# Kernel optimization log

Measured on AMD Instinct MI355X. Metric: run time of the kernel, lower is better.

The kernel has to match this reference:

```python
import jax, jax.numpy as jnp
import numpy as np

B, CHANS, SAMPLES = 256, 22, 1125
DEPTH, CD1, CD2, KT = 9, 24, 9, 75
K_CHEB, N_CHEB_LAYERS, AVEPOOL = 3, 5, 5
W1 = SAMPLES - KT + 1          # 1051 after valid (1,75) conv
WP = W1 // AVEPOOL             # 210 after avgpool
FEAT = CD2 * WP                # 1890 -> fc1


def _bn(x, p, eps=1e-5):
    # eval-mode BatchNorm2d over channel axis 1; p rows = [gamma, beta, mean, var]
    g, b, m, v = p
    s = (1, -1, 1, 1)
    return (x - m.reshape(s)) / jnp.sqrt(v.reshape(s) + eps) * g.reshape(s) + b.reshape(s)


def _normalize_A(A, lmax=2.0):
    A = jax.nn.relu(A)
    n = A.shape[0]
    I = jnp.eye(n, dtype=A.dtype)
    A = A * (1.0 - I)            # zero diagonal
    A = A + A.T                  # symmetrize
    d = jnp.sum(A, axis=1)
    dis = 1.0 / jnp.sqrt(d + 1e-10)
    L = I - dis[:, None] * A * dis[None, :]
    return 2.0 * L / lmax - I


def _forward(x, channel_weight, tconv1_w, bn1, tconv2_w, bn2, da_w, da_b,
             cconv1_w, bn3, A, A_mask, cheby_W, cheby_b, cconv2_w, bn4,
             fc1_w, fc1_b, mlp_w1, mlp_b1, mlp_w2, mlp_b2):
    dn = ('NCHW', 'OIHW', 'NCHW')
    # lead weighting: (B,1,C,S) x (H,1,C) -> (B,H,C,S)
    x = jnp.einsum('bdcw,hdc->bhcw', x, channel_weight)
    # time_conv: pointwise 1x1 + BN + depthwise (1,KT) + BN + GELU
    x = jnp.einsum('bicw,oi->bocw', x, tconv1_w)
    x = _bn(x, bn1)
    x = jax.lax.conv_general_dilated(x, tconv2_w.reshape(CD1, 1, 1, KT), (1, 1),
                                     'VALID', feature_group_count=CD1,
                                     dimension_numbers=dn)
    x = jax.nn.gelu(_bn(x, bn2), approximate=False)
    # EEGDepthAttention: avg over chans, (7,1) conv on depth axis, softmax over depth
    xp = jnp.mean(x, axis=2, keepdims=True)        # (B,CD1,1,W1)
    xt = jnp.swapaxes(xp, 1, 2)                    # (B,1,CD1,W1)
    y = jax.lax.conv_general_dilated(xt, da_w.reshape(1, 1, 7, 1), (1, 1),
                                     ((3, 3), (0, 0)), dimension_numbers=dn)
    y = jax.nn.softmax(y + da_b.reshape(1, 1, 1, 1), axis=-2)
    x = jnp.swapaxes(y, 1, 2) * CHANS * x          # (B,CD1,C,W1)
    # channel conv part1: 1x1 + BN -> (B,CD2,C,W1)
    x = _bn(jnp.einsum('bicw,oi->bocw', x, cconv1_w), bn3)
    # normalized Laplacian from pruned learnable adjacency
    L = _normalize_A(A * jax.nn.sigmoid(A_mask))
    I = jnp.eye(CHANS, dtype=L.dtype)
    adjs = [I, L, 2.0 * (L @ L) - I][:K_CHEB]      # Chebyshev T_0..T_2
    b_, f_, c_, w_ = x.shape
    xr = jnp.transpose(x, (0, 3, 1, 2)).reshape(b_ * w_, f_, c_)  # (N,F,C)
    for l in range(N_CHEB_LAYERS):
        out = jnp.zeros_like(xr)
        for k in range(K_CHEB):
            out = out + jnp.einsum('cd,nfd,fo->noc', adjs[k], xr, cheby_W[l, k]) \
                      + cheby_b[l, k][None, :, None]
        xr = jax.nn.relu(out)
    x = jnp.transpose(xr.reshape(b_, w_, f_, c_), (0, 2, 3, 1))   # (B,CD2,C,W1)
    # channel conv part2: depthwise (CHANS,1) + BN + GELU -> (B,CD2,1,W1)
    x = jnp.einsum('bfcw,fc->bfw', x, cconv2_w)[:, :, None, :]
    x = jax.nn.gelu(_bn(x, bn4), approximate=False)
    # avgpool kernel/stride AVEPOOL on time; dropout is identity at eval
    x = x[..., :WP * AVEPOOL].reshape(b_, CD2, 1, WP, AVEPOOL).mean(-1)
    x = x.reshape(b_, -1)                           # (B,FEAT)
    x = x @ fc1_w + fc1_b                           # (B,5)
    x = jax.nn.elu(x @ mlp_w1 + mlp_b1) @ mlp_w2 + mlp_b2
    return jax.nn.softmax(x, axis=1)


def setup_inputs() -> dict:
    key = jax.random.key(0)
    ks = iter(jax.random.split(key, 40))

    def randn(shape, s=1.0):
        return jax.random.normal(next(ks), shape, jnp.float32) * s

    def bn_p(c):
        return jnp.stack([jax.random.uniform(next(ks), (c,)) * 0.5 + 0.75,
                          randn((c,), 0.1), randn((c,), 0.1),
                          jax.random.uniform(next(ks), (c,)) * 0.5 + 0.75])

    return {
        'x': randn((B, 1, CHANS, SAMPLES)),
        'channel_weight': randn((DEPTH, 1, CHANS), 0.3),
        'tconv1_w': randn((CD1, DEPTH), 0.3),
        'bn1': bn_p(CD1),
        'tconv2_w': randn((CD1, KT), 0.1),
        'bn2': bn_p(CD1),
        'da_w': randn((7,), 0.3),
        'da_b': randn((1,), 0.1),
        'cconv1_w': randn((CD2, CD1), 0.2),
        'bn3': bn_p(CD2),
        'A': jax.random.uniform(next(ks), (CHANS, CHANS)) * 0.49 + 0.01,
        'A_mask': jnp.ones((CHANS, CHANS), jnp.float32),
        'cheby_W': randn((N_CHEB_LAYERS, K_CHEB, CD2, CD2), 0.3),
        'cheby_b': jnp.zeros((N_CHEB_LAYERS, K_CHEB, CD2), jnp.float32),
        'cconv2_w': randn((CD2, CHANS), 0.2),
        'bn4': bn_p(CD2),
        'fc1_w': randn((FEAT, 5), 0.02),
        'fc1_b': jnp.zeros((5,), jnp.float32),
        'mlp_w1': randn((5, 64), 0.3),
        'mlp_b1': jnp.zeros((64,), jnp.float32),
        'mlp_w2': randn((64, 4), 0.2),
        'mlp_b2': jnp.zeros((4,), jnp.float32),
    }


def reference(x, channel_weight, tconv1_w, bn1, tconv2_w, bn2, da_w, da_b,
              cconv1_w, bn3, A, A_mask, cheby_W, cheby_b, cconv2_w, bn4,
              fc1_w, fc1_b, mlp_w1, mlp_b1, mlp_w2, mlp_b2):
    return _forward(x, channel_weight, tconv1_w, bn1, tconv2_w, bn2, da_w, da_b,
                    cconv1_w, bn3, A, A_mask, cheby_W, cheby_b, cconv2_w, bn4,
                    fc1_w, fc1_b, mlp_w1, mlp_b1, mlp_w2, mlp_b2)
```

## Files before the change

kernel.cpp:

```cpp
#include <hip/hip_runtime.h>
#include <math.h>

#define B_      256
#define CHANS   22
#define SAMPLES 1125
#define DEPTH   9
#define CD1     24
#define CD2     9
#define KT      75
#define W1      1051
#define WP      210
#define FEAT    1890
#define TW      11
#define NT      96

#define WS_W2   0
#define WS_D    528
#define WS_CC1  552
#define WS_B3   768
#define WS_L1   777
#define WS_L2   1261
#define WS_CC2  1745
#define WS_B4   1943
#define WS_BL   1952
#define WS_KT   2000
#define WS_Z    3840

__device__ __forceinline__ float gelu_exact(float v) {
    return 0.5f * v * (1.0f + erff(v * 0.70710678118654752f));
}

__global__ __launch_bounds__(256) void precompute_kernel(
    const float* __restrict__ cw, const float* __restrict__ t1w,
    const float* __restrict__ bn1, const float* __restrict__ t2w,
    const float* __restrict__ bn2, const float* __restrict__ cc1w,
    const float* __restrict__ bn3, const float* __restrict__ A,
    const float* __restrict__ Am, const float* __restrict__ cbB,
    const float* __restrict__ cc2w, const float* __restrict__ bn4,
    float* __restrict__ ws)
{
    __shared__ float a1[CD1], a2[CD1];
    __shared__ float a3[CD2], a4[CD2];
    __shared__ float Ap[484], As[484], dis[22], L1s[484];
    const int tid = threadIdx.x;

    if (tid < CD1) {
        float g1 = bn1[tid], be1 = bn1[24 + tid], m1 = bn1[48 + tid], v1 = bn1[72 + tid];
        a1[tid] = g1 * rsqrtf(v1 + 1e-5f);
        float b1v = be1 - m1 * a1[tid];
        float g2 = bn2[tid], be2 = bn2[24 + tid], m2 = bn2[48 + tid], v2 = bn2[72 + tid];
        a2[tid] = g2 * rsqrtf(v2 + 1e-5f);
        float b2v = be2 - m2 * a2[tid];
        float S = 0.0f;
        for (int k = 0; k < KT; ++k) S += t2w[tid * KT + k];
        ws[WS_D + tid] = a2[tid] * b1v * S + b2v;
    }
    if (tid < CD2) {
        float g3 = bn3[tid], be3 = bn3[9 + tid], m3 = bn3[18 + tid], v3 = bn3[27 + tid];
        a3[tid] = g3 * rsqrtf(v3 + 1e-5f);
        ws[WS_B3 + tid] = be3 - m3 * a3[tid];
        float g4 = bn4[tid], be4 = bn4[9 + tid], m4 = bn4[18 + tid], v4 = bn4[27 + tid];
        a4[tid] = g4 * rsqrtf(v4 + 1e-5f);
        ws[WS_B4 + tid] = be4 - m4 * a4[tid];
    }
    __syncthreads();

    for (int e = tid; e < CD1 * CHANS; e += blockDim.x) {
        int o = e / CHANS, c = e - o * CHANS;
        float m = 0.0f;
        for (int h = 0; h < DEPTH; ++h) m += t1w[o * DEPTH + h] * cw[h * CHANS + c];
        ws[WS_W2 + e] = a2[o] * a1[o] * m;
    }
    for (int e = tid; e < CD2 * CD1; e += blockDim.x) {
        int o = e / CD1;
        ws[WS_CC1 + e] = a3[o] * cc1w[e] * 22.0f;
    }
    for (int e = tid; e < CD2 * CHANS; e += blockDim.x) {
        int f = e / CHANS;
        ws[WS_CC2 + e] = a4[f] * cc2w[e];
    }
    for (int e = tid; e < 45; e += blockDim.x) {
        int l = e / 9, o = e - l * 9;
        ws[WS_BL + e] = cbB[(l * 3 + 0) * 9 + o] + cbB[(l * 3 + 1) * 9 + o] + cbB[(l * 3 + 2) * 9 + o];
    }
    for (int e = tid; e < KT * CD1; e += blockDim.x) {
        int k = e / CD1, o = e - k * CD1;
        ws[WS_KT + e] = t2w[o * KT + k];
    }
    for (int e = tid; e < 484; e += blockDim.x) {
        int c = e / 22, d = e - c * 22;
        float v = A[e] / (1.0f + expf(-Am[e]));
        v = fmaxf(v, 0.0f);
        if (c == d) v = 0.0f;
        Ap[e] = v;
    }
    __syncthreads();
    for (int e = tid; e < 484; e += blockDim.x) {
        int c = e / 22, d = e - c * 22;
        As[e] = Ap[e] + Ap[d * 22 + c];
    }
    __syncthreads();
    if (tid < 22) {
        float s = 0.0f;
        for (int d = 0; d < 22; ++d) s += As[tid * 22 + d];
        dis[tid] = rsqrtf(s + 1e-10f);
    }
    __syncthreads();
    for (int e = tid; e < 484; e += blockDim.x) {
        int c = e / 22, d = e - c * 22;
        float v = -dis[c] * As[e] * dis[d];
        L1s[e] = v;
        ws[WS_L1 + e] = v;
    }
    __syncthreads();
    for (int e = tid; e < 484; e += blockDim.x) {
        int c = e / 22, d = e - c * 22;
        float s = 0.0f;
        for (int k2 = 0; k2 < 22; ++k2) s += L1s[c * 22 + k2] * L1s[k2 * 22 + d];
        ws[WS_L2 + e] = 2.0f * s - (c == d ? 1.0f : 0.0f);
    }
}

#define OXS  0
#define OX   0
#define XSTR 268
#define OG   2948
#define GSTR 532
#define OS   8800
#define XP   9088
#define SMEM_F 9360

__global__ __launch_bounds__(256, 4) void main_kernel(
    const float* __restrict__ x, const float* __restrict__ t2w,
    const float* __restrict__ daw_g, const float* __restrict__ dab_g,
    const float* __restrict__ cbW, float* __restrict__ ws)
{
    __shared__ float sm[SMEM_F];
    const int tid = threadIdx.x;
    const int b = blockIdx.y;
    const int w0 = blockIdx.x * TW;
    const float* cst = ws;
    float* zbuf = ws + WS_Z;

    const int c = tid / TW;
    const int t = tid - c * TW;
    const bool act = (tid < 242);

    for (int e = tid; e < 22 * 88; e += 256) {
        int ch = e / 88, j = e - ch * 88;
        int s = w0 + j;
        float v = 0.0f;
        if (j < 85 && s < SAMPLES) v = x[(b * CHANS + ch) * SAMPLES + s];
        sm[OXS + e] = v;
    }
    __syncthreads();

    if (act) {
        float acc[CD1];
        #pragma unroll
        for (int o = 0; o < CD1; ++o) acc[o] = 0.0f;
        const int xbase = OXS + c * 88 + t;
        #pragma unroll 1
        for (int kc = 0; kc < 9; ++kc) {
            float xw[8];
            #pragma unroll
            for (int j = 0; j < 8; ++j) xw[j] = sm[xbase + kc * 8 + j];
            const float* Ktc = cst + WS_KT + kc * 8 * CD1;
            #pragma unroll
            for (int j = 0; j < 8; ++j) {
                #pragma unroll
                for (int o = 0; o < CD1; ++o)
                    acc[o] = fmaf(Ktc[j * CD1 + o], xw[j], acc[o]);
            }
        }
        {
            float xw[3];
            #pragma unroll
            for (int j = 0; j < 3; ++j) xw[j] = sm[xbase + 72 + j];
            const float* Ktc = cst + WS_KT + 72 * CD1;
            #pragma unroll
            for (int j = 0; j < 3; ++j) {
                #pragma unroll
                for (int o = 0; o < CD1; ++o)
                    acc[o] = fmaf(Ktc[j * CD1 + o], xw[j], acc[o]);
            }
        }
        float g[CD1];
        #pragma unroll
        for (int o = 0; o < CD1; ++o) {
            float w2 = cst[WS_W2 + o * CHANS + c];
            float dd = cst[WS_D + o];
            g[o] = gelu_exact(fmaf(w2, acc[o], dd));
        }
        float4* gp = (float4*)&sm[OG + t * GSTR + c * 24];
        #pragma unroll
        for (int q = 0; q < 6; ++q)
            gp[q] = make_float4(g[4 * q], g[4 * q + 1], g[4 * q + 2], g[4 * q + 3]);
    }
    __syncthreads();

    for (int e = tid; e < CD1 * TW; e += 256) {
        int d = e / TW, tt = e - d * TW;
        float s = 0.0f;
        #pragma unroll
        for (int ch = 0; ch < CHANS; ++ch) s += sm[OG + tt * GSTR + ch * 24 + d];
        sm[XP + e] = s * (1.0f / 22.0f);
    }
    __syncthreads();
    for (int e = tid; e < CD1 * TW; e += 256) {
        int d = e / TW, tt = e - d * TW;
        float y = dab_g[0];
        #pragma unroll
        for (int j = 0; j < 7; ++j) {
            int dd = d + j - 3;
            if (dd >= 0 && dd < CD1) y += daw_g[j] * sm[XP + dd * TW + tt];
        }
        sm[OS + d * 12 + tt] = y;
    }
    __syncthreads();
    if (tid < TW) {
        float mx = -1e30f;
        for (int d = 0; d < CD1; ++d) mx = fmaxf(mx, sm[OS + d * 12 + tid]);
        float sum = 0.0f;
        for (int d = 0; d < CD1; ++d) {
            float e2 = expf(sm[OS + d * 12 + tid] - mx);
            sm[OS + d * 12 + tid] = e2;
            sum += e2;
        }
        float inv = 1.0f / sum;
        for (int d = 0; d < CD1; ++d) sm[OS + d * 12 + tid] *= inv;
    }
    __syncthreads();

    float xo[CD2];
    if (act) {
        float garr[CD1];
        {
            const float4* gp = (const float4*)&sm[OG + t * GSTR + c * 24];
            #pragma unroll
            for (int q = 0; q < 6; ++q) {
                float4 v = gp[q];
                garr[4 * q] = v.x; garr[4 * q + 1] = v.y;
                garr[4 * q + 2] = v.z; garr[4 * q + 3] = v.w;
            }
        }
        #pragma unroll
        for (int o = 0; o < CD2; ++o) xo[o] = cst[WS_B3 + o];
        #pragma unroll
        for (int i = 0; i < CD1; ++i) {
            float s = sm[OS + i * 12 + t];
            float p = s * garr[i];
            #pragma unroll
            for (int o = 0; o < CD2; ++o)
                xo[o] = fmaf(cst[WS_CC1 + o * CD1 + i], p, xo[o]);
        }
        float4* xp = (float4*)&sm[OX + t * XSTR + c * 12];
        xp[0] = make_float4(xo[0], xo[1], xo[2], xo[3]);
        xp[1] = make_float4(xo[4], xo[5], xo[6], xo[7]);
        xp[2] = make_float4(xo[8], 0.0f, 0.0f, 0.0f);
    }
    __syncthreads();

    float t1row[CHANS], t2row[CHANS];
    if (act) {
        #pragma unroll
        for (int d = 0; d < CHANS; ++d) {
            t1row[d] = cst[WS_L1 + c * 22 + d];
            t2row[d] = cst[WS_L2 + c * 22 + d];
        }
    }

    for (int l = 0; l < 5; ++l) {
        float y1[CD2], y2[CD2];
        if (act) {
            #pragma unroll
            for (int o = 0; o < CD2; ++o) { y1[o] = 0.0f; y2[o] = 0.0f; }
            #pragma unroll
            for (int d = 0; d < CHANS; ++d) {
                const float4* p = (const float4*)&sm[OX + t * XSTR + d * 12];
                float4 a = p[0], bb = p[1];
                float x8 = sm[OX + t * XSTR + d * 12 + 8];
                float w1c = t1row[d], w2c = t2row[d];
                y1[0] = fmaf(w1c, a.x, y1[0]);  y2[0] = fmaf(w2c, a.x, y2[0]);
                y1[1] = fmaf(w1c, a.y, y1[1]);  y2[1] = fmaf(w2c, a.y, y2[1]);
                y1[2] = fmaf(w1c, a.z, y1[2]);  y2[2] = fmaf(w2c, a.z, y2[2]);
                y1[3] = fmaf(w1c, a.w, y1[3]);  y2[3] = fmaf(w2c, a.w, y2[3]);
                y1[4] = fmaf(w1c, bb.x, y1[4]); y2[4] = fmaf(w2c, bb.x, y2[4]);
                y1[5] = fmaf(w1c, bb.y, y1[5]); y2[5] = fmaf(w2c, bb.y, y2[5]);
                y1[6] = fmaf(w1c, bb.z, y1[6]); y2[6] = fmaf(w2c, bb.z, y2[6]);
                y1[7] = fmaf(w1c, bb.w, y1[7]); y2[7] = fmaf(w2c, bb.w, y2[7]);
                y1[8] = fmaf(w1c, x8, y1[8]);   y2[8] = fmaf(w2c, x8, y2[8]);
            }
            float out[CD2];
            #pragma unroll
            for (int o = 0; o < CD2; ++o) out[o] = cst[WS_BL + l * 9 + o];
            #pragma unroll
            for (int f = 0; f < CD2; ++f) {
                const float* w0p = cbW + ((l * 3 + 0) * 9 + f) * 9;
                const float* w1p = cbW + ((l * 3 + 1) * 9 + f) * 9;
                const float* w2p = cbW + ((l * 3 + 2) * 9 + f) * 9;
                float xv = xo[f], yv1 = y1[f], yv2 = y2[f];
                #pragma unroll
                for (int o = 0; o < CD2; ++o)
                    out[o] = fmaf(w0p[o], xv, fmaf(w1p[o], yv1, fmaf(w2p[o], yv2, out[o])));
            }
            #pragma unroll
            for (int o = 0; o < CD2; ++o) xo[o] = fmaxf(out[o], 0.0f);
        }
        __syncthreads();
        if (act) {
            float4* xp = (float4*)&sm[OX + t * XSTR + c * 12];
            xp[0] = make_float4(xo[0], xo[1], xo[2], xo[3]);
            xp[1] = make_float4(xo[4], xo[5], xo[6], xo[7]);
            xp[2] = make_float4(xo[8], 0.0f, 0.0f, 0.0f);
        }
        __syncthreads();
    }

    if (tid < CD2 * TW) {
        int f = tid / TW, tt = tid - f * TW;
        float a = cst[WS_B4 + f];
        #pragma unroll
        for (int ch = 0; ch < CHANS; ++ch)
            a = fmaf(cst[WS_CC2 + f * CHANS + ch], sm[OX + tt * XSTR + ch * 12 + f], a);
        float z = gelu_exact(a);
        int w = w0 + tt;
        if (w < W1) zbuf[(b * CD2 + f) * W1 + w] = z;
    }
}

__global__ __launch_bounds__(256) void head_kernel(
    const float* __restrict__ ws, const float* __restrict__ fc1w,
    const float* __restrict__ fc1b, const float* __restrict__ w1,
    const float* __restrict__ b1, const float* __restrict__ w2,
    const float* __restrict__ b2, float* __restrict__ out)
{
    __shared__ float red[5][256];
    __shared__ float l5[5];
    __shared__ float hbuf[64];
    const int tid = threadIdx.x;
    const int b = blockIdx.x;
    const float* zb = ws + WS_Z + b * CD2 * W1;

    float part[5] = {0, 0, 0, 0, 0};
    for (int i = tid; i < FEAT; i += 256) {
        int f = i / WP, t = i - f * WP;
        const float* zp = zb + f * W1 + 5 * t;
        float pooled = 0.2f * (zp[0] + zp[1] + zp[2] + zp[3] + zp[4]);
        #pragma unroll
        for (int j = 0; j < 5; ++j) part[j] = fmaf(pooled, fc1w[i * 5 + j], part[j]);
    }
    #pragma unroll
    for (int j = 0; j < 5; ++j) red[j][tid] = part[j];
    __syncthreads();
    for (int ofs = 128; ofs > 0; ofs >>= 1) {
        if (tid < ofs) {
            #pragma unroll
            for (int j = 0; j < 5; ++j) red[j][tid] += red[j][tid + ofs];
        }
        __syncthreads();
    }
    if (tid < 5) l5[tid] = red[tid][0] + fc1b[tid];
    __syncthreads();
    if (tid < 64) {
        float a = b1[tid];
        #pragma unroll
        for (int j = 0; j < 5; ++j) a = fmaf(l5[j], w1[j * 64 + tid], a);
        hbuf[tid] = (a > 0.0f) ? a : expm1f(a);
    }
    __syncthreads();
    if (tid == 0) {
        float o4[4];
        #pragma unroll
        for (int m = 0; m < 4; ++m) {
            float a = b2[m];
            for (int k = 0; k < 64; ++k) a = fmaf(hbuf[k], w2[k * 4 + m], a);
            o4[m] = a;
        }
        float mx = fmaxf(fmaxf(o4[0], o4[1]), fmaxf(o4[2], o4[3]));
        float s = 0.0f;
        #pragma unroll
        for (int m = 0; m < 4; ++m) { o4[m] = expf(o4[m] - mx); s += o4[m]; }
        float inv = 1.0f / s;
        #pragma unroll
        for (int m = 0; m < 4; ++m) out[b * 4 + m] = o4[m] * inv;
    }
}

extern "C" void kernel_launch(void* const* d_in, const int* in_sizes, int n_in,
                              void* d_out, int out_size, void* d_ws, size_t ws_size,
                              hipStream_t stream)
{
    const float* x    = (const float*)d_in[0];
    const float* cw   = (const float*)d_in[1];
    const float* t1w  = (const float*)d_in[2];
    const float* bn1  = (const float*)d_in[3];
    const float* t2w  = (const float*)d_in[4];
    const float* bn2  = (const float*)d_in[5];
    const float* daw  = (const float*)d_in[6];
    const float* dab  = (const float*)d_in[7];
    const float* cc1w = (const float*)d_in[8];
    const float* bn3  = (const float*)d_in[9];
    const float* A    = (const float*)d_in[10];
    const float* Am   = (const float*)d_in[11];
    const float* cbW  = (const float*)d_in[12];
    const float* cbB  = (const float*)d_in[13];
    const float* cc2w = (const float*)d_in[14];
    const float* bn4  = (const float*)d_in[15];
    const float* fc1w = (const float*)d_in[16];
    const float* fc1b = (const float*)d_in[17];
    const float* w1   = (const float*)d_in[18];
    const float* b1   = (const float*)d_in[19];
    const float* w2   = (const float*)d_in[20];
    const float* b2   = (const float*)d_in[21];
    float* ws  = (float*)d_ws;
    float* out = (float*)d_out;

    hipLaunchKernelGGL(precompute_kernel, dim3(1), dim3(256), 0, stream,
                       cw, t1w, bn1, t2w, bn2, cc1w, bn3, A, Am, cbB, cc2w, bn4, ws);
    hipLaunchKernelGGL(main_kernel, dim3(NT, B_), dim3(256), 0, stream,
                       x, t2w, daw, dab, cbW, ws);
    hipLaunchKernelGGL(head_kernel, dim3(B_), dim3(256), 0, stream,
                       ws, fc1w, fc1b, w1, b1, w2, b2, out);
}
```

Before: 936.8 us.

## Compute depthwise temporal conv with bf16 MFMA and fast polynomial GELU

Replaces the per-thread scalar FMA loop for the 75-tap temporal convolution with bf16 MFMA 16x16x32 instructions. The convolution weights are pre-converted to a padded bf16 matrix, and the input window is staged in LDS as bf16, with a shifted copy so odd-offset fragments stay aligned. Exact erf GELU is replaced by an Abramowitz-Stegun polynomial approximation that uses hardware rcp and exp2. This cuts the VALU work in the dominant conv stage, at the cost of bf16 input and weight precision and an approximate GELU, which may affect numerical tolerance.

```diff
diff --git a/kernel.cpp b/kernel.cpp
--- a/kernel.cpp
+++ b/kernel.cpp
@@ -1,4 +1,5 @@
 #include <hip/hip_runtime.h>
+#include <hip/hip_bf16.h>
 #include <math.h>
 
 #define B_      256
@@ -14,7 +15,6 @@
 #define TW      11
 #define NT      96
 
-#define WS_W2   0
 #define WS_D    528
 #define WS_CC1  552
 #define WS_B3   768
@@ -23,11 +23,22 @@
 #define WS_CC2  1745
 #define WS_B4   1943
 #define WS_BL   1952
-#define WS_KT   2000
-#define WS_Z    3840
-
-__device__ __forceinline__ float gelu_exact(float v) {
-    return 0.5f * v * (1.0f + erff(v * 0.70710678118654752f));
+#define WS_W2T  2000
+#define WS_KTB  2528
+#define WS_Z    4096
+
+typedef short short8 __attribute__((ext_vector_type(8)));
+typedef float f32x4  __attribute__((ext_vector_type(4)));
+
+__device__ __forceinline__ float gelu_fast(float v) {
+    float u = v * 0.70710678118654752f;
+    float s = fabsf(u);
+    float t = __builtin_amdgcn_rcpf(fmaf(0.3275911f, s, 1.0f));
+    float p = fmaf(fmaf(fmaf(fmaf(1.061405429f, t, -1.453152027f), t,
+                             1.421413741f), t, -0.284496736f), t, 0.254829592f) * t;
+    float e = __builtin_amdgcn_exp2f(s * s * -1.4426950408889634f);
+    float er = copysignf(fmaf(-p, e, 1.0f), u);
+    return fmaf(0.5f * v, er, 0.5f * v);
 }
 
 __global__ __launch_bounds__(256) void precompute_kernel(
@@ -65,11 +76,19 @@
     }
     __syncthreads();
 
-    for (int e = tid; e < CD1 * CHANS; e += blockDim.x) {
-        int o = e / CHANS, c = e - o * CHANS;
+    for (int e = tid; e < CHANS * 24; e += blockDim.x) {
+        int c = e / 24, o = e - c * 24;
         float m = 0.0f;
         for (int h = 0; h < DEPTH; ++h) m += t1w[o * DEPTH + h] * cw[h * CHANS + c];
-        ws[WS_W2 + e] = a2[o] * a1[o] * m;
+        ws[WS_W2T + e] = a2[o] * a1[o] * m;
+    }
+    {
+        __hip_bfloat16* ktb = (__hip_bfloat16*)(ws + WS_KTB);
+        for (int e = tid; e < 32 * 96; e += blockDim.x) {
+            int o = e / 96, k = e - o * 96;
+            float v = (o < CD1 && k < KT) ? t2w[o * KT + k] : 0.0f;
+            ktb[e] = __float2bfloat16(v);
+        }
     }
     for (int e = tid; e < CD2 * CD1; e += blockDim.x) {
         int o = e / CD1;
@@ -82,10 +101,6 @@
     for (int e = tid; e < 45; e += blockDim.x) {
         int l = e / 9, o = e - l * 9;
         ws[WS_BL + e] = cbB[(l * 3 + 0) * 9 + o] + cbB[(l * 3 + 1) * 9 + o] + cbB[(l * 3 + 2) * 9 + o];
-    }
-    for (int e = tid; e < KT * CD1; e += blockDim.x) {
-        int k = e / CD1, o = e - k * CD1;
-        ws[WS_KT + e] = t2w[o * KT + k];
     }
     for (int e = tid; e < 484; e += blockDim.x) {
         int c = e / 22, d = e - c * 22;
@@ -121,7 +136,6 @@
     }
 }
 
-#define OXS  0
 #define OX   0
 #define XSTR 268
 #define OG   2948
@@ -142,60 +156,69 @@
     const float* cst = ws;
     float* zbuf = ws + WS_Z;
 
-    const int c = tid / TW;
-    const int t = tid - c * TW;
-    const bool act = (tid < 242);
-
-    for (int e = tid; e < 22 * 88; e += 256) {
-        int ch = e / 88, j = e - ch * 88;
-        int s = w0 + j;
-        float v = 0.0f;
-        if (j < 85 && s < SAMPLES) v = x[(b * CHANS + ch) * SAMPLES + s];
-        sm[OXS + e] = v;
-    }
-    __syncthreads();
-
-    if (act) {
-        float acc[CD1];
-        #pragma unroll
-        for (int o = 0; o < CD1; ++o) acc[o] = 0.0f;
-        const int xbase = OXS + c * 88 + t;
-        #pragma unroll 1
-        for (int kc = 0; kc < 9; ++kc) {
-            float xw[8];
-            #pragma unroll
-            for (int j = 0; j < 8; ++j) xw[j] = sm[xbase + kc * 8 + j];
-            const float* Ktc = cst + WS_KT + kc * 8 * CD1;
-            #pragma unroll
-            for (int j = 0; j < 8; ++j) {
-                #pragma unroll
-                for (int o = 0; o < CD1; ++o)
-                    acc[o] = fmaf(Ktc[j * CD1 + o], xw[j], acc[o]);
+    const int lane = tid & 63;
+    const int wid  = tid >> 6;
+    const int quad = lane >> 4;
+    const int lt   = lane & 15;
+
+    {
+        __hip_bfloat16* xbuf = (__hip_bfloat16*)sm;
+        for (int e = tid; e < 22 * 112; e += 256) {
+            int ch = e / 112, j = e - ch * 112;
+            int s = w0 + j;
+            float v = (j < 85 && s < SAMPLES) ? x[(b * CHANS + ch) * SAMPLES + s] : 0.0f;
+            __hip_bfloat16 h = __float2bfloat16(v);
+            xbuf[e] = h;
+            if (j > 0) xbuf[2464 + e - 1] = h;
+            if (j == 111) xbuf[2464 + e] = __float2bfloat16(0.0f);
+        }
+    }
+    __syncthreads();
+
+    {
+        short8 afr0[3], afr1[3];
+        const short* ktb = (const short*)(cst + WS_KTB);
+        #pragma unroll
+        for (int kt = 0; kt < 3; ++kt) {
+            afr0[kt] = *(const short8*)(ktb + lt * 96 + kt * 32 + quad * 8);
+            afr1[kt] = *(const short8*)(ktb + (lt + 16) * 96 + kt * 32 + quad * 8);
+        }
+        const int xebase = (lt & 1) ? (2464 - 1 + lt) : lt;
+        const int* smi = (const int*)sm;
+
+        for (int c = wid; c < CHANS; c += 4) {
+            f32x4 acc0 = {0.f, 0.f, 0.f, 0.f}, acc1 = {0.f, 0.f, 0.f, 0.f};
+            #pragma unroll
+            for (int kt = 0; kt < 3; ++kt) {
+                int bi = (xebase + c * 112 + quad * 8 + kt * 32) >> 1;
+                union { int i[4]; short8 s; } B;
+                B.i[0] = smi[bi];     B.i[1] = smi[bi + 1];
+                B.i[2] = smi[bi + 2]; B.i[3] = smi[bi + 3];
+                acc0 = __builtin_amdgcn_mfma_f32_16x16x32_bf16(afr0[kt], B.s, acc0, 0, 0, 0);
+                acc1 = __builtin_amdgcn_mfma_f32_16x16x32_bf16(afr1[kt], B.s, acc1, 0, 0, 0);
             }
-        }
-        {
-            float xw[3];
-            #pragma unroll
-            for (int j = 0; j < 3; ++j) xw[j] = sm[xbase + 72 + j];
-            const float* Ktc = cst + WS_KT + 72 * CD1;
-            #pragma unroll
-            for (int j = 0; j < 3; ++j) {
-                #pragma unroll
-                for (int o = 0; o < CD1; ++o)
-                    acc[o] = fmaf(Ktc[j * CD1 + o], xw[j], acc[o]);
+            const int t = lt;
+            if (t < TW) {
+                {
+                    const float* w2p = cst + WS_W2T + c * 24 + quad * 4;
+                    const float* ddp = cst + WS_D + quad * 4;
+                    float g0 = gelu_fast(fmaf(w2p[0], acc0[0], ddp[0]));
+                    float g1 = gelu_fast(fmaf(w2p[1], acc0[1], ddp[1]));
+                    float g2 = gelu_fast(fmaf(w2p[2], acc0[2], ddp[2]));
+                    float g3 = gelu_fast(fmaf(w2p[3], acc0[3], ddp[3]));
+                    *(float4*)&sm[OG + t * GSTR + c * 24 + quad * 4] = make_float4(g0, g1, g2, g3);
+                }
+                if (quad < 2) {
+                    const float* w2p = cst + WS_W2T + c * 24 + 16 + quad * 4;
+                    const float* ddp = cst + WS_D + 16 + quad * 4;
+                    float g0 = gelu_fast(fmaf(w2p[0], acc1[0], ddp[0]));
+                    float g1 = gelu_fast(fmaf(w2p[1], acc1[1], ddp[1]));
+                    float g2 = gelu_fast(fmaf(w2p[2], acc1[2], ddp[2]));
+                    float g3 = gelu_fast(fmaf(w2p[3], acc1[3], ddp[3]));
+                    *(float4*)&sm[OG + t * GSTR + c * 24 + 16 + quad * 4] = make_float4(g0, g1, g2, g3);
+                }
             }
         }
-        float g[CD1];
-        #pragma unroll
-        for (int o = 0; o < CD1; ++o) {
-            float w2 = cst[WS_W2 + o * CHANS + c];
-            float dd = cst[WS_D + o];
-            g[o] = gelu_exact(fmaf(w2, acc[o], dd));
-        }
-        float4* gp = (float4*)&sm[OG + t * GSTR + c * 24];
-        #pragma unroll
-        for (int q = 0; q < 6; ++q)
-            gp[q] = make_float4(g[4 * q], g[4 * q + 1], g[4 * q + 2], g[4 * q + 3]);
     }
     __syncthreads();
 
@@ -231,6 +254,10 @@
         for (int d = 0; d < CD1; ++d) sm[OS + d * 12 + tid] *= inv;
     }
     __syncthreads();
+
+    const int c = tid / TW;
+    const int t = tid - c * TW;
+    const bool act = (tid < 242);
 
     float xo[CD2];
     if (act) {
@@ -323,7 +350,7 @@
         #pragma unroll
         for (int ch = 0; ch < CHANS; ++ch)
             a = fmaf(cst[WS_CC2 + f * CHANS + ch], sm[OX + tt * XSTR + ch * 12 + f], a);
-        float z = gelu_exact(a);
+        float z = gelu_fast(a);
         int w = w0 + tt;
         if (w < W1) zbuf[(b * CD2 + f) * W1 + w] = z;
     }
```

Result: faster. 884.2 us (-5.6%).
